# Kernel optimization log

Measured on AMD Instinct MI355X. Metric: run time of the kernel, lower is better.

## Reference

```python
import jax, jax.numpy as jnp
import numpy as np

B, T, C, H = 128, 256, 256, 8
HS = C // H  # 32
EPS = 1e-5


def _layernorm(x, g, b):
    mu = jnp.mean(x, axis=-1, keepdims=True)
    var = jnp.mean(jnp.square(x - mu), axis=-1, keepdims=True)
    return g * (x - mu) / jnp.sqrt(var + EPS) + b


def setup_inputs() -> dict:
    key = jax.random.key(0)
    ks = jax.random.split(key, 12)
    s = 0.02
    return {
        "x": jax.random.normal(ks[0], (B, T, C), dtype=jnp.float32),
        "Wk": jax.random.normal(ks[1], (H, C, HS), dtype=jnp.float32) * s,
        "Wq": jax.random.normal(ks[2], (H, C, HS), dtype=jnp.float32) * s,
        "Wv": jax.random.normal(ks[3], (H, C, HS), dtype=jnp.float32) * s,
        "Wp": jax.random.normal(ks[4], (C, C), dtype=jnp.float32) * s,
        "bp": jnp.zeros((C,), dtype=jnp.float32),
        "W1": jax.random.normal(ks[5], (C, 4 * C), dtype=jnp.float32) * s,
        "b1": jnp.zeros((4 * C,), dtype=jnp.float32),
        "W2": jax.random.normal(ks[6], (4 * C, C), dtype=jnp.float32) * s,
        "b2": jnp.zeros((C,), dtype=jnp.float32),
        "g1": jnp.ones((C,), dtype=jnp.float32),
        "be1": jnp.zeros((C,), dtype=jnp.float32),
        "g2": jnp.ones((C,), dtype=jnp.float32),
        "be2": jnp.zeros((C,), dtype=jnp.float32),
    }


def reference(x, Wk, Wq, Wv, Wp, bp, W1, b1, W2, b2, g1, be1, g2, be2):
    Bx, Tx, Cx = x.shape
    # --- multi-head self-attention on ln1(x) ---
    h = _layernorm(x, g1, be1)
    k = jnp.einsum('btc,hcd->bhtd', h, Wk)
    q = jnp.einsum('btc,hcd->bhtd', h, Wq)
    v = jnp.einsum('btc,hcd->bhtd', h, Wv)
    # NOTE: source computes k @ q^T (transposed vs standard) and scales by C**-0.5
    scores = jnp.einsum('bhtd,bhsd->bhts', k, q) * (Cx ** -0.5)
    mask = jnp.tril(jnp.ones((Tx, Tx), dtype=bool))  # causal lower-triangular
    scores = jnp.where(mask, scores, -jnp.inf)
    w = jax.nn.softmax(scores, axis=-1)
    o = jnp.einsum('bhts,bhsd->bhtd', w, v)
    o = o.transpose(0, 2, 1, 3).reshape(Bx, Tx, Cx)  # concat heads
    x = x + (o @ Wp + bp)
    # --- feed-forward (swish) on ln2(x) ---
    h2 = _layernorm(x, g2, be2)
    f = h2 @ W1 + b1
    f = f * jax.nn.sigmoid(f)  # swish
    f = f @ W2 + b2
    return x + f
```

## Files before the change

kernel.cpp:

```cpp
#include <hip/hip_runtime.h>
#include <cstdint>

#define BB 128
#define TT 256
#define CC 256
#define HH 8
#define HSZ 32
#define NT (BB*TT)
#define CF (4*CC)
#define LN_EPS 1e-5f
#define SCALE 0.0625f

typedef __attribute__((ext_vector_type(8))) __bf16 bf16x8;
typedef __attribute__((ext_vector_type(4))) float f32x4;
typedef __attribute__((ext_vector_type(16))) float f32x16;
typedef __attribute__((ext_vector_type(2))) long i64x2;
typedef unsigned short u16;
typedef unsigned int u32;
typedef unsigned char u8;

__device__ __forceinline__ u16 f2bf(float f) {
  u32 u = __float_as_uint(f);
  u32 r = (u + 0x7fffu + ((u >> 16) & 1u)) >> 16;
  return (u16)r;
}
__device__ __forceinline__ u8 f2f8(float f) {
  return (u8)(__builtin_amdgcn_cvt_pk_fp8_f32(f, f, 0, false) & 0xff);
}
__device__ __forceinline__ u32 f2f8x4(float a, float b, float c, float d) {
  u32 pk = (u32)__builtin_amdgcn_cvt_pk_fp8_f32(a, b, 0, false);
  return (u32)__builtin_amdgcn_cvt_pk_fp8_f32(c, d, (int)pk, true);
}
__device__ __forceinline__ uint2 f2bfx4(float a, float b, float c, float d) {
  uint2 r;
  asm("v_cvt_pk_bf16_f32 %0, %1, %2" : "=v"(r.x) : "v"(a), "v"(b));
  asm("v_cvt_pk_bf16_f32 %0, %1, %2" : "=v"(r.y) : "v"(c), "v"(d));
  return r;
}
__device__ __forceinline__ int swz3i(int r) { return (r ^ (r >> 2)) & 3; }
__device__ __forceinline__ int pkrow(int row, int k) {
  int g = (k >> 4) & 3, h = (k >> 3) & 1, j = k & 7;
  int c = (h << 1) + (g >> 1);
  int cp = c ^ swz3i(row);
  return (k & ~63) + cp * 16 + ((g & 1) << 3) + j;
}

__device__ __forceinline__ void gload16(const void* g, void* l) {
  __builtin_amdgcn_global_load_lds(
      (const __attribute__((address_space(1))) u32*)(uintptr_t)g,
      (__attribute__((address_space(3))) u32*)(u32)(uintptr_t)l,
      16, 0, 0);
}

__device__ __forceinline__ void wait_vm0() {
  asm volatile("s_waitcnt vmcnt(0)" ::: "memory");
  __builtin_amdgcn_sched_barrier(0);
}
__device__ __forceinline__ void wait_vm4() {
  asm volatile("s_waitcnt vmcnt(4)" ::: "memory");
  __builtin_amdgcn_sched_barrier(0);
}
__device__ __forceinline__ void wait_vm8() {
  asm volatile("s_waitcnt vmcnt(8)" ::: "memory");
  __builtin_amdgcn_sched_barrier(0);
}
__device__ __forceinline__ void wait_vm0_lgkm0() {
  asm volatile("s_waitcnt vmcnt(0) lgkmcnt(0)" ::: "memory");
  __builtin_amdgcn_sched_barrier(0);
}
__device__ __forceinline__ void wait_lgkm0() {
  asm volatile("s_waitcnt lgkmcnt(0)" ::: "memory");
  __builtin_amdgcn_sched_barrier(0);
}
__device__ __forceinline__ void sbar() {
  __builtin_amdgcn_s_barrier();
  __builtin_amdgcn_sched_barrier(0);
}

__global__ __launch_bounds__(256) void conv_ln(
    const float* __restrict__ Wk, const float* __restrict__ Wq,
    const float* __restrict__ Wv, const float* __restrict__ Wp,
    const float* __restrict__ W1, const float* __restrict__ W2,
    u8* __restrict__ WkqvT8, u8* __restrict__ WpT8,
    u8* __restrict__ W1T8, u8* __restrict__ W2T8,
    const float* __restrict__ x, const float* __restrict__ g1,
    const float* __restrict__ be1, u8* __restrict__ hb) {
  __shared__ u8 ldsT[64][68];
  int bid = blockIdx.x, tid = threadIdx.x;
  if (bid >= 192) {
    int wid = tid >> 6, lane = tid & 63;
    int row = (bid - 192) * 4 + wid;
    const float4 v = reinterpret_cast<const float4*>(x + (size_t)row * CC)[lane];
    float s = v.x + v.y + v.z + v.w;
#pragma unroll
    for (int o = 32; o; o >>= 1) s += __shfl_xor(s, o, 64);
    float mu = s * (1.0f / CC);
    float dx = v.x - mu, dy = v.y - mu, dz = v.z - mu, dw = v.w - mu;
    float ss = dx * dx + dy * dy + dz * dz + dw * dw;
#pragma unroll
    for (int o = 32; o; o >>= 1) ss += __shfl_xor(ss, o, 64);
    float inv = rsqrtf(ss * (1.0f / CC) + LN_EPS);
    const float4 gv = reinterpret_cast<const float4*>(g1)[lane];
    const float4 bv = reinterpret_cast<const float4*>(be1)[lane];
    u32 pk = f2f8x4(gv.x * dx * inv + bv.x, gv.y * dy * inv + bv.y,
                    gv.z * dz * inv + bv.z, gv.w * dw * inv + bv.w);
    *reinterpret_cast<u32*>(hb + (size_t)row * CC + pkrow(row, lane * 4)) = pk;
    return;
  }
  int n0, k0, K;
  u8* dst;
  int mode;
  const float* src = nullptr;
  int sk = 0;
  if (bid < 48) {
    mode = 0; n0 = (bid >> 2) * 64; k0 = (bid & 3) * 64; K = 256; dst = WkqvT8;
  } else if (bid < 112) {
    int l = bid - 48;
    mode = 1; n0 = (l >> 2) * 64; k0 = (l & 3) * 64; K = 256; dst = W1T8;
    src = W1; sk = 1024;
  } else if (bid < 176) {
    int l = bid - 112;
    mode = 1; n0 = (l >> 4) * 64; k0 = (l & 15) * 64; K = 1024; dst = W2T8;
    src = W2; sk = 256;
  } else {
    int l = bid - 176;
    mode = 1; n0 = (l >> 2) * 64; k0 = (l & 3) * 64; K = 256; dst = WpT8;
    src = Wp; sk = 256;
  }
  int kr = tid >> 2;
  int nbase = (tid & 3) * 16;
#pragma unroll
  for (int u = 0; u < 4; ++u) {
    int nl = nbase + u * 4;
    int ng = n0 + nl;
    float4 v;
    if (mode == 0) {
      const float* W = (ng < 256) ? Wk : (ng < 512 ? Wq : Wv);
      int inner = ng & 255;
      v = *reinterpret_cast<const float4*>(
          &W[((inner >> 5) << 13) + (size_t)(k0 + kr) * 32 + (inner & 31)]);
    } else {
      v = *reinterpret_cast<const float4*>(
          &src[(size_t)(k0 + kr) * sk + ng]);
    }
    ldsT[nl + 0][kr] = f2f8(v.x);
    ldsT[nl + 1][kr] = f2f8(v.y);
    ldsT[nl + 2][kr] = f2f8(v.z);
    ldsT[nl + 3][kr] = f2f8(v.w);
  }
  __syncthreads();
  int nl = tid >> 2;
  int nglob = n0 + nl;
  int sz = swz3i(nglob);
  u8* drow = dst + (size_t)nglob * K + k0;
#pragma unroll
  for (int c4 = (tid & 3) * 4; c4 < (tid & 3) * 4 + 4; ++c4) {
    int q = c4 >> 1, s = c4 & 1;
    int kb = q * 8 + s * 4;
    u32 pk = (u32)ldsT[nl][kb] | ((u32)ldsT[nl][kb + 1] << 8) |
             ((u32)ldsT[nl][kb + 2] << 16) | ((u32)ldsT[nl][kb + 3] << 24);
    int g = (kb >> 4) & 3, h8 = (kb >> 3) & 1;
    int cp = ((h8 << 1) + (g >> 1)) ^ sz;
    *reinterpret_cast<u32*>(drow + cp * 16 + ((g & 1) << 3) + (kb & 7)) = pk;
  }
}

template <int NB>
__global__ __launch_bounds__(512, 4) void panel_fused(
    const u8* __restrict__ Asrc, const u8* __restrict__ WT8,
    void* __restrict__ outp, int N) {
  __shared__ u8 Bw[4][256][64];
  int tid = threadIdx.x;
  int w = tid >> 6, lane = tid & 63;
  int l32 = lane & 31, h = lane >> 5;
  int th = w >> 2, fq = w & 3;
  int m0 = blockIdx.x * 64;

#define STAGEP(nb)                                                            \
  {                                                                           \
    _Pragma("unroll") for (int it = 0; it < 8; ++it) {                        \
      int f = it * 512 + tid;                                                 \
      int kg = f >> 10, t = (f >> 2) & 255, c = f & 3;                        \
      gload16(WT8 + (size_t)((nb) * 256 + t) * 256 + kg * 64 + c * 16,        \
              &Bw[0][0][0] + f * 16);                                         \
    }                                                                         \
  }
  i64x2 aa[4][2];
  {
    int ar = th * 32 + l32;
    int az = swz3i(ar);
#pragma unroll
    for (int kg = 0; kg < 4; ++kg)
#pragma unroll
      for (int p = 0; p < 2; ++p)
        aa[kg][p] = *reinterpret_cast<const i64x2*>(
            Asrc + (size_t)(m0 + ar) * 256 + kg * 64 +
            ((((h << 1) + p) ^ az) << 4));
  }
  STAGEP(0);

#pragma unroll 1
  for (int nb = 0; nb < NB; ++nb) {
    if (nb == 0) wait_vm0(); else wait_vm8();
    sbar();
    f32x16 a1[2] = {};
    __builtin_amdgcn_s_setprio(1);
#pragma unroll
    for (int kg = 0; kg < 4; ++kg) {
#pragma unroll
      for (int p = 0; p < 2; ++p) {
        i64x2 bB[2];
#pragma unroll
        for (int j = 0; j < 2; ++j) {
          int br = fq * 64 + j * 32 + l32, bz = swz3i(br);
          bB[j] = *reinterpret_cast<const i64x2*>(
              &Bw[kg][br][(((h << 1) + p) ^ bz) << 4]);
        }
#pragma unroll
        for (int j = 0; j < 2; ++j) {
          a1[j] = __builtin_amdgcn_mfma_f32_32x32x16_fp8_fp8(
              bB[j][0], aa[kg][p][0], a1[j], 0, 0, 0);
          a1[j] = __builtin_amdgcn_mfma_f32_32x32x16_fp8_fp8(
              bB[j][1], aa[kg][p][1], a1[j], 0, 0, 0);
        }
      }
    }
    __builtin_amdgcn_s_setprio(0);
    sbar();
    if (nb < NB - 1) STAGEP(nb + 1);
    int m = m0 + th * 32 + l32;
#pragma unroll
    for (int j = 0; j < 2; ++j) {
#pragma unroll
      for (int q = 0; q < 4; ++q) {
        int n = nb * 256 + fq * 64 + j * 32 + q * 8 + h * 4;
        size_t off = (size_t)m * N + n;
        u16 pk[4];
#pragma unroll
        for (int r = 0; r < 4; ++r) pk[r] = f2bf(a1[j][q * 4 + r]);
        *reinterpret_cast<uint2*>(&((u16*)outp)[off]) =
            *reinterpret_cast<uint2*>(pk);
      }
    }
  }
#undef STAGEP
}

__global__ __launch_bounds__(512, 4) void wp_ffn(
    const u8* __restrict__ o8, const u8* __restrict__ WpT8,
    const float* __restrict__ bp, const float* __restrict__ x,
    const u8* __restrict__ W1T8, const u8* __restrict__ W2T8,
    const float* __restrict__ b1, const float* __restrict__ b2,
    const float* __restrict__ g2, const float* __restrict__ be2,
    u8* __restrict__ hb, float* __restrict__ outp) {
  __shared__ u8 Bw[65536];
  __shared__ u8 Ff[2][64][64];
  __shared__ float b1l[1024];
  __shared__ float red[4][64][2];
  int tid = threadIdx.x;
  int w = tid >> 6, lane = tid & 63;
  int l32 = lane & 31, h = lane >> 5;
  int th = w >> 2, fq = w & 3;
  int m0 = blockIdx.x * 64;
  int m = m0 + th * 32 + l32;
  int ar = th * 32 + l32, az = swz3i(ar);

#define STAGE_W1F(nb)                                                         \
  {                                                                           \
    _Pragma("unroll") for (int it = 0; it < 4; ++it) {                        \
      int f = it * 512 + tid;                                                 \
      int kg = f >> 9, t = (f >> 2) & 127, c = f & 3;                         \
      gload16(W1T8 + (size_t)((nb) * 128 + t) * 256 + kg * 64 + c * 16,       \
              Bw + f * 16);                                                   \
    }                                                                         \
  }
#define STAGE_W2F(nb)                                                         \
  {                                                                           \
    _Pragma("unroll") for (int it = 0; it < 4; ++it) {                        \
      int f = it * 512 + tid;                                                 \
      int kg2 = f >> 10, o = (f >> 2) & 255, c = f & 3;                       \
      gload16(W2T8 + (size_t)o * 1024 + (nb) * 128 + kg2 * 64 + c * 16,       \
              Bw + 32768 + f * 16);                                           \
    }                                                                         \
  }

  i64x2 aw[4][2];
#pragma unroll
  for (int kg = 0; kg < 4; ++kg)
#pragma unroll
    for (int p = 0; p < 2; ++p)
      aw[kg][p] = *reinterpret_cast<const i64x2*>(
          o8 + (size_t)(m0 + ar) * 256 + kg * 64 + ((((h << 1) + p) ^ az) << 4));
  {
#pragma unroll
    for (int it = 0; it < 8; ++it) {
      int f = it * 512 + tid;
      int kg = f >> 10, t = (f >> 2) & 255, c = f & 3;
      gload16(WpT8 + (size_t)t * 256 + kg * 64 + c * 16, Bw + f * 16);
    }
  }
  float4 xr[8];
#pragma unroll
  for (int j = 0; j < 2; ++j)
#pragma unroll
    for (int q = 0; q < 4; ++q) {
      int n = fq * 64 + j * 32 + q * 8 + h * 4;
      xr[j * 4 + q] = *reinterpret_cast<const float4*>(&x[(size_t)m * 256 + n]);
    }
  wait_vm0();
  sbar();
  f32x16 xw[2] = {};
  __builtin_amdgcn_s_setprio(1);
#pragma unroll
  for (int kg = 0; kg < 4; ++kg) {
#pragma unroll
    for (int p = 0; p < 2; ++p) {
      i64x2 bB[2];
#pragma unroll
      for (int j = 0; j < 2; ++j) {
        int br = fq * 64 + j * 32 + l32, bz = swz3i(br);
        bB[j] = *reinterpret_cast<const i64x2*>(
            &Bw[kg * 16384 + br * 64 + ((((h << 1) + p) ^ bz) << 4)]);
      }
#pragma unroll
      for (int j = 0; j < 2; ++j) {
        xw[j] = __builtin_amdgcn_mfma_f32_32x32x16_fp8_fp8(
            bB[j][0], aw[kg][p][0], xw[j], 0, 0, 0);
        xw[j] = __builtin_amdgcn_mfma_f32_32x32x16_fp8_fp8(
            bB[j][1], aw[kg][p][1], xw[j], 0, 0, 0);
      }
    }
  }
  __builtin_amdgcn_s_setprio(0);
  sbar();
  STAGE_W1F(0);
  STAGE_W2F(0);
  if (w < 4) gload16(b1 + (size_t)(w * 256 + lane * 4), b1l + w * 256 + lane * 4);
  float s1 = 0.f, s2 = 0.f;
#pragma unroll
  for (int j = 0; j < 2; ++j) {
#pragma unroll
    for (int q = 0; q < 4; ++q) {
      int n = fq * 64 + j * 32 + q * 8 + h * 4;
      const float4 bv = *reinterpret_cast<const float4*>(&bp[n]);
      const float4 rv = xr[j * 4 + q];
      float o0 = xw[j][q * 4 + 0] + bv.x + rv.x;
      float o1 = xw[j][q * 4 + 1] + bv.y + rv.y;
      float o2 = xw[j][q * 4 + 2] + bv.z + rv.z;
      float o3 = xw[j][q * 4 + 3] + bv.w + rv.w;
      xw[j][q * 4 + 0] = o0; xw[j][q * 4 + 1] = o1;
      xw[j][q * 4 + 2] = o2; xw[j][q * 4 + 3] = o3;
      s1 += (o0 + o1) + (o2 + o3);
      s2 += (o0 * o0 + o1 * o1) + (o2 * o2 + o3 * o3);
    }
  }
  s1 += __shfl_xor(s1, 32, 64);
  s2 += __shfl_xor(s2, 32, 64);
  if (h == 0) { red[fq][ar][0] = s1; red[fq][ar][1] = s2; }
  wait_lgkm0();
  sbar();
  {
    float S1 = (red[0][ar][0] + red[1][ar][0]) + (red[2][ar][0] + red[3][ar][0]);
    float S2 = (red[0][ar][1] + red[1][ar][1]) + (red[2][ar][1] + red[3][ar][1]);
    float mu = S1 * (1.0f / 256.0f);
    float inv = rsqrtf(fmaxf(S2 * (1.0f / 256.0f) - mu * mu, 0.0f) + LN_EPS);
#pragma unroll
    for (int j = 0; j < 2; ++j) {
#pragma unroll
      for (int q = 0; q < 4; ++q) {
        int n = fq * 64 + j * 32 + q * 8 + h * 4;
        const float4 gv = *reinterpret_cast<const float4*>(&g2[n]);
        const float4 bb = *reinterpret_cast<const float4*>(&be2[n]);
        u32 pk = f2f8x4(gv.x * (xw[j][q * 4 + 0] - mu) * inv + bb.x,
                        gv.y * (xw[j][q * 4 + 1] - mu) * inv + bb.y,
                        gv.z * (xw[j][q * 4 + 2] - mu) * inv + bb.z,
                        gv.w * (xw[j][q * 4 + 3] - mu) * inv + bb.w);
        *reinterpret_cast<u32*>(hb + (size_t)m * 256 + pkrow(m, n)) = pk;
      }
    }
  }
  wait_vm0();
  sbar();
  i64x2 aa[4][2];
#pragma unroll
  for (int kg = 0; kg < 4; ++kg)
#pragma unroll
    for (int p = 0; p < 2; ++p)
      aa[kg][p] = *reinterpret_cast<const i64x2*>(
          hb + (size_t)(m0 + ar) * 256 + kg * 64 + ((((h << 1) + p) ^ az) << 4));

  f32x16 acc2[2] = {};
#pragma unroll 1
  for (int nb = 0; nb < 8; ++nb) {
    wait_vm4();
    sbar();
    f32x16 a1 = {};
    __builtin_amdgcn_s_setprio(1);
#pragma unroll
    for (int kg = 0; kg < 4; ++kg) {
      int br = fq * 32 + l32, bz = swz3i(br);
#pragma unroll
      for (int p = 0; p < 2; ++p) {
        i64x2 bB = *reinterpret_cast<const i64x2*>(
            &Bw[kg * 8192 + br * 64 + ((((h << 1) + p) ^ bz) << 4)]);
        a1 = __builtin_amdgcn_mfma_f32_32x32x16_fp8_fp8(
            bB[0], aa[kg][p][0], a1, 0, 0, 0);
        a1 = __builtin_amdgcn_mfma_f32_32x32x16_fp8_fp8(
            bB[1], aa[kg][p][1], a1, 0, 0, 0);
      }
    }
    __builtin_amdgcn_s_setprio(0);
    int kg2w = fq >> 1;
    {
      int tz = swz3i(ar);
#pragma unroll
      for (int q = 0; q < 4; ++q) {
        int g = (fq & 1) * 2 + (q >> 1);
        int hh = q & 1;
        int c = (hh << 1) + (g >> 1);
        const float4 bv = *reinterpret_cast<const float4*>(
            &b1l[nb * 128 + fq * 32 + q * 8 + h * 4]);
        float bf[4] = {bv.x, bv.y, bv.z, bv.w};
        float sv[4];
#pragma unroll
        for (int r = 0; r < 4; ++r) {
          float fv = a1[q * 4 + r] + bf[r];
          float e = __builtin_amdgcn_exp2f(fv * -1.44269504f);
          sv[r] = fv * __builtin_amdgcn_rcpf(1.0f + e);
        }
        *reinterpret_cast<u32*>(
            &Ff[kg2w][ar][((c ^ tz) << 4) + ((g & 1) << 3) + h * 4]) =
            f2f8x4(sv[0], sv[1], sv[2], sv[3]);
      }
    }
    wait_vm0_lgkm0();
    sbar();
    if (nb < 7) STAGE_W1F(nb + 1);
    __builtin_amdgcn_s_setprio(1);
#pragma unroll
    for (int kg2 = 0; kg2 < 2; ++kg2)
#pragma unroll
      for (int p = 0; p < 2; ++p) {
        i64x2 fa = *reinterpret_cast<const i64x2*>(
            &Ff[kg2][ar][(((h << 1) + p) ^ swz3i(ar)) << 4]);
        i64x2 bb2[2];
#pragma unroll
        for (int j = 0; j < 2; ++j) {
          int br = fq * 64 + j * 32 + l32;
          bb2[j] = *reinterpret_cast<const i64x2*>(
              &Bw[32768 + kg2 * 16384 + br * 64 +
                  ((((h << 1) + p) ^ swz3i(br)) << 4)]);
        }
#pragma unroll
        for (int j = 0; j < 2; ++j) {
          acc2[j] = __builtin_amdgcn_mfma_f32_32x32x16_fp8_fp8(
              bb2[j][0], fa[0], acc2[j], 0, 0, 0);
          acc2[j] = __builtin_amdgcn_mfma_f32_32x32x16_fp8_fp8(
              bb2[j][1], fa[1], acc2[j], 0, 0, 0);
        }
      }
    __builtin_amdgcn_s_setprio(0);
    sbar();
    if (nb < 7) STAGE_W2F(nb + 1);
  }
#undef STAGE_W1F
#undef STAGE_W2F
#pragma unroll
  for (int j = 0; j < 2; ++j) {
#pragma unroll
    for (int q = 0; q < 4; ++q) {
      int n = fq * 64 + j * 32 + q * 8 + h * 4;
      size_t off = (size_t)m * 256 + n;
      const float4 bv = *reinterpret_cast<const float4*>(&b2[n]);
      float4 o;
      o.x = acc2[j][q * 4 + 0] + bv.x + xw[j][q * 4 + 0];
      o.y = acc2[j][q * 4 + 1] + bv.y + xw[j][q * 4 + 1];
      o.z = acc2[j][q * 4 + 2] + bv.z + xw[j][q * 4 + 2];
      o.w = acc2[j][q * 4 + 3] + bv.w + xw[j][q * 4 + 3];
      *reinterpret_cast<float4*>(&outp[off]) = o;
    }
  }
}

__global__ __launch_bounds__(256) void attn_kernel(const u16* __restrict__ kqv,
                                                   u8* __restrict__ o8) {
  __shared__ u16 q_lds[256 * 32];
  __shared__ u16 vT[32 * 256];
  __shared__ u16 pT[4 * 16 * 64];
  int bh = blockIdx.x;
  int b = bh >> 3, h = bh & 7;
  int tid = threadIdx.x, wid = tid >> 6, lane = tid & 63;
  int l16 = lane & 15, lh = lane >> 4;
  const size_t rowbase = (size_t)b * TT * 768;
  {
    int sr = tid >> 2, c = tid & 3;
    for (int s = sr; s < 256; s += 64) {
      uint4 qv = *reinterpret_cast<const uint4*>(
          &kqv[rowbase + (size_t)s * 768 + 256 + h * 32 + c * 8]);
      *reinterpret_cast<uint4*>((char*)q_lds + ((s * 64 + c * 16) ^ ((s & 7) << 4))) = qv;
      u16 tmp[8];
      *reinterpret_cast<uint4*>(tmp) = *reinterpret_cast<const uint4*>(
          &kqv[rowbase + (size_t)s * 768 + 512 + h * 32 + c * 8]);
#pragma unroll
      for (int e = 0; e < 8; ++e) {
        int d = c * 8 + e;
        vT[d * 256 + (((s >> 3) ^ ((d >> 1) & 7)) << 3) + (s & 7)] = tmp[e];
      }
    }
  }
  __syncthreads();
  u16* pw = &pT[wid * 16 * 64];
  const float C1 = 0.09016844f;
  for (int j = 0; j < 4; ++j) {
    int t16 = (j * 4 + wid) * 16;
    bf16x8 kb = *reinterpret_cast<const bf16x8*>(
        &kqv[rowbase + (size_t)(t16 + l16) * 768 + h * 32 + lh * 8]);
    float m2 = -3e38f, lsum = 0.f;
    f32x4 oacc[2] = {};
    for (int st = 0; st <= j; ++st) {
      int s0 = st << 6;
      float v[4][4];
      float pm[4];
#pragma unroll
      for (int sj = 0; sj < 4; ++sj) {
        int srow = s0 + sj * 16 + l16;
        bf16x8 qa = *reinterpret_cast<const bf16x8*>(
            (char*)q_lds + ((srow * 64 + lh * 16) ^ ((srow & 7) << 4)));
        f32x4 z = {0.f, 0.f, 0.f, 0.f};
        f32x4 sc = __builtin_amdgcn_mfma_f32_16x16x32_bf16(qa, kb, z, 0, 0, 0);
#pragma unroll
        for (int r = 0; r < 4; ++r) {
          float val = sc[r];
          if (st == j) {
            if (sj * 16 + lh * 4 + r > wid * 16 + l16) val = -3e38f;
          }
          v[sj][r] = val;
        }
        pm[sj] = fmaxf(fmaxf(v[sj][0], v[sj][1]), fmaxf(v[sj][2], v[sj][3]));
      }
      float mx = fmaxf(fmaxf(pm[0], pm[1]), fmaxf(pm[2], pm[3]));
      mx = fmaxf(mx, __shfl_xor(mx, 16, 64));
      mx = fmaxf(mx, __shfl_xor(mx, 32, 64));
      float mxs = mx * C1;
      if (!__all(mxs <= m2 + 8.0f)) {
        float mn = fmaxf(m2, mxs);
        float alpha = exp2f(m2 - mn);
        m2 = mn;
        lsum *= alpha;
#pragma unroll
        for (int r = 0; r < 4; ++r) {
          float a = __shfl(alpha, (lane & 48) | (lh * 4 + r), 64);
          oacc[0][r] *= a;
          oacc[1][r] *= a;
        }
      }
#pragma unroll
      for (int sj = 0; sj < 4; ++sj) {
        float p0 = exp2f(__builtin_fmaf(v[sj][0], C1, -m2));
        float p1 = exp2f(__builtin_fmaf(v[sj][1], C1, -m2));
        float p2 = exp2f(__builtin_fmaf(v[sj][2], C1, -m2));
        float p3 = exp2f(__builtin_fmaf(v[sj][3], C1, -m2));
        lsum += (p0 + p1) + (p2 + p3);
        uint2 pkv = f2bfx4(p0, p1, p2, p3);
        *reinterpret_cast<uint2*>(
            (char*)pw + ((l16 * 128 + sj * 32 + lh * 8) ^ ((l16 & 7) << 4))) = pkv;
      }
#pragma unroll
      for (int ks = 0; ks < 2; ++ks) {
        bf16x8 pa = *reinterpret_cast<const bf16x8*>(
            (char*)pw + ((l16 * 128 + ks * 64 + lh * 16) ^ ((l16 & 7) << 4)));
#pragma unroll
        for (int nI = 0; nI < 2; ++nI) {
          int d = nI * 16 + l16;
          int sch = ((s0 + ks * 32 + lh * 8) >> 3) ^ ((d >> 1) & 7);
          bf16x8 vb = *reinterpret_cast<const bf16x8*>(&vT[d * 256 + (sch << 3)]);
          oacc[nI] = __builtin_amdgcn_mfma_f32_16x16x32_bf16(pa, vb, oacc[nI], 0, 0, 0);
        }
      }
    }
    lsum += __shfl_xor(lsum, 16, 64);
    lsum += __shfl_xor(lsum, 32, 64);
#pragma unroll
    for (int r = 0; r < 4; ++r) {
      float ls = __shfl(lsum, (lane & 48) | (lh * 4 + r), 64);
      float inv = 1.0f / ls;
      int t = t16 + lh * 4 + r;
      size_t rb = (size_t)(b * TT + t) * CC;
#pragma unroll
      for (int nI = 0; nI < 2; ++nI) {
        int c = h * HSZ + nI * 16 + l16;
        o8[rb + pkrow(t, c)] = f2f8(oacc[nI][r] * inv);
      }
    }
  }
}

extern "C" void kernel_launch(void* const* d_in, const int* in_sizes, int n_in,
                              void* d_out, int out_size, void* d_ws, size_t ws_size,
                              hipStream_t stream) {
  const float* x   = (const float*)d_in[0];
  const float* Wk  = (const float*)d_in[1];
  const float* Wq  = (const float*)d_in[2];
  const float* Wv  = (const float*)d_in[3];
  const float* Wp  = (const float*)d_in[4];
  const float* bp  = (const float*)d_in[5];
  const float* W1  = (const float*)d_in[6];
  const float* b1  = (const float*)d_in[7];
  const float* W2  = (const float*)d_in[8];
  const float* b2  = (const float*)d_in[9];
  const float* g1  = (const float*)d_in[10];
  const float* be1 = (const float*)d_in[11];
  const float* g2  = (const float*)d_in[12];
  const float* be2 = (const float*)d_in[13];

  char* ws = (char*)d_ws;
  u16* kqv = (u16*)(ws + 0);
  u8*  o8  = (u8*)(ws + 50331648);
  u8*  hb  = (u8*)(ws + 100663296);
  char* wb = ws + 117440512;
  u8*  WkqvT8 = (u8*)(wb);
  u8*  WpT8   = (u8*)(wb + 196608);
  u8*  W1T8   = (u8*)(wb + 196608 + 65536);
  u8*  W2T8   = (u8*)(wb + 196608 + 65536 + 262144);

  conv_ln<<<192 + NT / 4, 256, 0, stream>>>(Wk, Wq, Wv, Wp, W1, W2,
                                            WkqvT8, WpT8, W1T8, W2T8,
                                            x, g1, be1, hb);
  panel_fused<3><<<NT / 64, 512, 0, stream>>>(hb, WkqvT8, kqv, 768);
  attn_kernel<<<BB * HH, 256, 0, stream>>>(kqv, o8);
  wp_ffn<<<NT / 64, 512, 0, stream>>>(o8, WpT8, bp, x, W1T8, W2T8,
                                      b1, b2, g2, be2, hb, (float*)d_out);
}
```

Before: 127.4 us.

## Process two query tiles per wave in attention to share Q/V LDS loads

The attention kernel now handles query tiles in pairs (jA, jB) inside one fully unrolled loop. Each Q fragment and V fragment read from LDS feeds MFMAs for both tiles, and the two independent online-softmax chains interleave to expose more instruction-level parallelism. The P scratch buffer doubles to hold one tile per pair member. Separately, the residual x load in the fused projection/MLP kernel moves from before the Wp MFMA loop to the epilogue, lowering register pressure at the cost of exposing that load's latency.

```diff
diff --git a/kernel.cpp b/kernel.cpp
--- a/kernel.cpp
+++ b/kernel.cpp
@@ -299,14 +299,6 @@
       gload16(WpT8 + (size_t)t * 256 + kg * 64 + c * 16, Bw + f * 16);
     }
   }
-  float4 xr[8];
-#pragma unroll
-  for (int j = 0; j < 2; ++j)
-#pragma unroll
-    for (int q = 0; q < 4; ++q) {
-      int n = fq * 64 + j * 32 + q * 8 + h * 4;
-      xr[j * 4 + q] = *reinterpret_cast<const float4*>(&x[(size_t)m * 256 + n]);
-    }
   wait_vm0();
   sbar();
   f32x16 xw[2] = {};
@@ -342,8 +334,9 @@
 #pragma unroll
     for (int q = 0; q < 4; ++q) {
       int n = fq * 64 + j * 32 + q * 8 + h * 4;
+      size_t off = (size_t)m * 256 + n;
       const float4 bv = *reinterpret_cast<const float4*>(&bp[n]);
-      const float4 rv = xr[j * 4 + q];
+      const float4 rv = *reinterpret_cast<const float4*>(&x[off]);
       float o0 = xw[j][q * 4 + 0] + bv.x + rv.x;
       float o1 = xw[j][q * 4 + 1] + bv.y + rv.y;
       float o2 = xw[j][q * 4 + 2] + bv.z + rv.z;
@@ -486,7 +479,7 @@
                                                    u8* __restrict__ o8) {
   __shared__ u16 q_lds[256 * 32];
   __shared__ u16 vT[32 * 256];
-  __shared__ u16 pT[4 * 16 * 64];
+  __shared__ u16 pT[8 * 16 * 64];
   int bh = blockIdx.x;
   int b = bh >> 3, h = bh & 7;
   int tid = threadIdx.x, wid = tid >> 6, lane = tid & 63;
@@ -509,87 +502,147 @@
     }
   }
   __syncthreads();
-  u16* pw = &pT[wid * 16 * 64];
+  u16* pwA = &pT[(wid * 2 + 0) * 16 * 64];
+  u16* pwB = &pT[(wid * 2 + 1) * 16 * 64];
   const float C1 = 0.09016844f;
-  for (int j = 0; j < 4; ++j) {
-    int t16 = (j * 4 + wid) * 16;
-    bf16x8 kb = *reinterpret_cast<const bf16x8*>(
-        &kqv[rowbase + (size_t)(t16 + l16) * 768 + h * 32 + lh * 8]);
-    float m2 = -3e38f, lsum = 0.f;
-    f32x4 oacc[2] = {};
-    for (int st = 0; st <= j; ++st) {
+#pragma unroll
+  for (int pp = 0; pp < 2; ++pp) {
+    const int jA = 2 * pp, jB = 2 * pp + 1;
+    int tA16 = (jA * 4 + wid) * 16, tB16 = (jB * 4 + wid) * 16;
+    bf16x8 kbA = *reinterpret_cast<const bf16x8*>(
+        &kqv[rowbase + (size_t)(tA16 + l16) * 768 + h * 32 + lh * 8]);
+    bf16x8 kbB = *reinterpret_cast<const bf16x8*>(
+        &kqv[rowbase + (size_t)(tB16 + l16) * 768 + h * 32 + lh * 8]);
+    float m2A = -3e38f, m2B = -3e38f, lsA = 0.f, lsB = 0.f;
+    f32x4 oA[2] = {}, oB[2] = {};
+#pragma unroll
+    for (int st = 0; st <= jB; ++st) {
+      const bool actA = (st <= jA);
       int s0 = st << 6;
-      float v[4][4];
-      float pm[4];
+      float vA[4][4], vB[4][4], pmA[4], pmB[4];
 #pragma unroll
       for (int sj = 0; sj < 4; ++sj) {
         int srow = s0 + sj * 16 + l16;
         bf16x8 qa = *reinterpret_cast<const bf16x8*>(
             (char*)q_lds + ((srow * 64 + lh * 16) ^ ((srow & 7) << 4)));
         f32x4 z = {0.f, 0.f, 0.f, 0.f};
-        f32x4 sc = __builtin_amdgcn_mfma_f32_16x16x32_bf16(qa, kb, z, 0, 0, 0);
+        f32x4 scB = __builtin_amdgcn_mfma_f32_16x16x32_bf16(qa, kbB, z, 0, 0, 0);
 #pragma unroll
         for (int r = 0; r < 4; ++r) {
-          float val = sc[r];
-          if (st == j) {
-            if (sj * 16 + lh * 4 + r > wid * 16 + l16) val = -3e38f;
+          float vb_ = scB[r];
+          if (st == jB) {
+            if (sj * 16 + lh * 4 + r > wid * 16 + l16) vb_ = -3e38f;
           }
-          v[sj][r] = val;
-        }
-        pm[sj] = fmaxf(fmaxf(v[sj][0], v[sj][1]), fmaxf(v[sj][2], v[sj][3]));
-      }
-      float mx = fmaxf(fmaxf(pm[0], pm[1]), fmaxf(pm[2], pm[3]));
-      mx = fmaxf(mx, __shfl_xor(mx, 16, 64));
-      mx = fmaxf(mx, __shfl_xor(mx, 32, 64));
-      float mxs = mx * C1;
-      if (!__all(mxs <= m2 + 8.0f)) {
-        float mn = fmaxf(m2, mxs);
-        float alpha = exp2f(m2 - mn);
-        m2 = mn;
-        lsum *= alpha;
-#pragma unroll
-        for (int r = 0; r < 4; ++r) {
-          float a = __shfl(alpha, (lane & 48) | (lh * 4 + r), 64);
-          oacc[0][r] *= a;
-          oacc[1][r] *= a;
-        }
-      }
-#pragma unroll
-      for (int sj = 0; sj < 4; ++sj) {
-        float p0 = exp2f(__builtin_fmaf(v[sj][0], C1, -m2));
-        float p1 = exp2f(__builtin_fmaf(v[sj][1], C1, -m2));
-        float p2 = exp2f(__builtin_fmaf(v[sj][2], C1, -m2));
-        float p3 = exp2f(__builtin_fmaf(v[sj][3], C1, -m2));
-        lsum += (p0 + p1) + (p2 + p3);
-        uint2 pkv = f2bfx4(p0, p1, p2, p3);
-        *reinterpret_cast<uint2*>(
-            (char*)pw + ((l16 * 128 + sj * 32 + lh * 8) ^ ((l16 & 7) << 4))) = pkv;
+          vB[sj][r] = vb_;
+        }
+        pmB[sj] = fmaxf(fmaxf(vB[sj][0], vB[sj][1]), fmaxf(vB[sj][2], vB[sj][3]));
+        if (actA) {
+          f32x4 scA = __builtin_amdgcn_mfma_f32_16x16x32_bf16(qa, kbA, z, 0, 0, 0);
+#pragma unroll
+          for (int r = 0; r < 4; ++r) {
+            float va_ = scA[r];
+            if (st == jA) {
+              if (sj * 16 + lh * 4 + r > wid * 16 + l16) va_ = -3e38f;
+            }
+            vA[sj][r] = va_;
+          }
+          pmA[sj] = fmaxf(fmaxf(vA[sj][0], vA[sj][1]), fmaxf(vA[sj][2], vA[sj][3]));
+        }
+      }
+      if (actA) {
+        float mx = fmaxf(fmaxf(pmA[0], pmA[1]), fmaxf(pmA[2], pmA[3]));
+        mx = fmaxf(mx, __shfl_xor(mx, 16, 64));
+        mx = fmaxf(mx, __shfl_xor(mx, 32, 64));
+        float mxs = mx * C1;
+        if (!__all(mxs <= m2A + 8.0f)) {
+          float mn = fmaxf(m2A, mxs);
+          float alpha = exp2f(m2A - mn);
+          m2A = mn;
+          lsA *= alpha;
+#pragma unroll
+          for (int r = 0; r < 4; ++r) {
+            float a = __shfl(alpha, (lane & 48) | (lh * 4 + r), 64);
+            oA[0][r] *= a;
+            oA[1][r] *= a;
+          }
+        }
+#pragma unroll
+        for (int sj = 0; sj < 4; ++sj) {
+          float p0 = exp2f(__builtin_fmaf(vA[sj][0], C1, -m2A));
+          float p1 = exp2f(__builtin_fmaf(vA[sj][1], C1, -m2A));
+          float p2 = exp2f(__builtin_fmaf(vA[sj][2], C1, -m2A));
+          float p3 = exp2f(__builtin_fmaf(vA[sj][3], C1, -m2A));
+          lsA += (p0 + p1) + (p2 + p3);
+          uint2 pkv = f2bfx4(p0, p1, p2, p3);
+          *reinterpret_cast<uint2*>(
+              (char*)pwA + ((l16 * 128 + sj * 32 + lh * 8) ^ ((l16 & 7) << 4))) = pkv;
+        }
+      }
+      {
+        float mx = fmaxf(fmaxf(pmB[0], pmB[1]), fmaxf(pmB[2], pmB[3]));
+        mx = fmaxf(mx, __shfl_xor(mx, 16, 64));
+        mx = fmaxf(mx, __shfl_xor(mx, 32, 64));
+        float mxs = mx * C1;
+        if (!__all(mxs <= m2B + 8.0f)) {
+          float mn = fmaxf(m2B, mxs);
+          float alpha = exp2f(m2B - mn);
+          m2B = mn;
+          lsB *= alpha;
+#pragma unroll
+          for (int r = 0; r < 4; ++r) {
+            float a = __shfl(alpha, (lane & 48) | (lh * 4 + r), 64);
+            oB[0][r] *= a;
+            oB[1][r] *= a;
+          }
+        }
+#pragma unroll
+        for (int sj = 0; sj < 4; ++sj) {
+          float p0 = exp2f(__builtin_fmaf(vB[sj][0], C1, -m2B));
+          float p1 = exp2f(__builtin_fmaf(vB[sj][1], C1, -m2B));
+          float p2 = exp2f(__builtin_fmaf(vB[sj][2], C1, -m2B));
+          float p3 = exp2f(__builtin_fmaf(vB[sj][3], C1, -m2B));
+          lsB += (p0 + p1) + (p2 + p3);
+          uint2 pkv = f2bfx4(p0, p1, p2, p3);
+          *reinterpret_cast<uint2*>(
+              (char*)pwB + ((l16 * 128 + sj * 32 + lh * 8) ^ ((l16 & 7) << 4))) = pkv;
+        }
       }
 #pragma unroll
       for (int ks = 0; ks < 2; ++ks) {
-        bf16x8 pa = *reinterpret_cast<const bf16x8*>(
-            (char*)pw + ((l16 * 128 + ks * 64 + lh * 16) ^ ((l16 & 7) << 4)));
+        bf16x8 paB = *reinterpret_cast<const bf16x8*>(
+            (char*)pwB + ((l16 * 128 + ks * 64 + lh * 16) ^ ((l16 & 7) << 4)));
+        bf16x8 paA;
+        if (actA)
+          paA = *reinterpret_cast<const bf16x8*>(
+              (char*)pwA + ((l16 * 128 + ks * 64 + lh * 16) ^ ((l16 & 7) << 4)));
 #pragma unroll
         for (int nI = 0; nI < 2; ++nI) {
           int d = nI * 16 + l16;
           int sch = ((s0 + ks * 32 + lh * 8) >> 3) ^ ((d >> 1) & 7);
           bf16x8 vb = *reinterpret_cast<const bf16x8*>(&vT[d * 256 + (sch << 3)]);
-          oacc[nI] = __builtin_amdgcn_mfma_f32_16x16x32_bf16(pa, vb, oacc[nI], 0, 0, 0);
-        }
-      }
-    }
-    lsum += __shfl_xor(lsum, 16, 64);
-    lsum += __shfl_xor(lsum, 32, 64);
+          if (actA)
+            oA[nI] = __builtin_amdgcn_mfma_f32_16x16x32_bf16(paA, vb, oA[nI], 0, 0, 0);
+          oB[nI] = __builtin_amdgcn_mfma_f32_16x16x32_bf16(paB, vb, oB[nI], 0, 0, 0);
+        }
+      }
+    }
+    lsA += __shfl_xor(lsA, 16, 64);
+    lsA += __shfl_xor(lsA, 32, 64);
+    lsB += __shfl_xor(lsB, 16, 64);
+    lsB += __shfl_xor(lsB, 32, 64);
 #pragma unroll
     for (int r = 0; r < 4; ++r) {
-      float ls = __shfl(lsum, (lane & 48) | (lh * 4 + r), 64);
-      float inv = 1.0f / ls;
-      int t = t16 + lh * 4 + r;
-      size_t rb = (size_t)(b * TT + t) * CC;
+      float laA = __shfl(lsA, (lane & 48) | (lh * 4 + r), 64);
+      float laB = __shfl(lsB, (lane & 48) | (lh * 4 + r), 64);
+      float invA = 1.0f / laA, invB = 1.0f / laB;
+      int tA = tA16 + lh * 4 + r, tB = tB16 + lh * 4 + r;
+      size_t rbA = (size_t)(b * TT + tA) * CC;
+      size_t rbB = (size_t)(b * TT + tB) * CC;
 #pragma unroll
       for (int nI = 0; nI < 2; ++nI) {
         int c = h * HSZ + nI * 16 + l16;
-        o8[rb + pkrow(t, c)] = f2f8(oacc[nI][r] * inv);
+        o8[rbA + pkrow(tA, c)] = f2f8(oA[nI][r] * invA);
+        o8[rbB + pkrow(tB, c)] = f2f8(oB[nI][r] * invB);
       }
     }
   }
```

Measured after the change: 125.1 us. Within noise of the previous version (-1.8%).
